# Optimization experiments

Measured on AMD Instinct MI355X. Metric: run time of the kernel, lower is better.

Reference implementation:

```python
import jax, jax.numpy as jnp
import numpy as np

B, SQ, SK, DK, DV = 16, 2048, 2048, 64, 64


def setup_inputs() -> dict:
    key = jax.random.key(0)
    kq, kk, kv, km = jax.random.split(key, 4)
    Q = jax.random.normal(kq, (B, SQ, DK), dtype=jnp.float32)
    K = jax.random.normal(kk, (B, SK, DK), dtype=jnp.float32)
    V = jax.random.normal(kv, (B, SK, DV), dtype=jnp.float32)
    mask = jax.random.randint(km, (B, 1, SK), 0, 2, dtype=jnp.int32)
    return {"Q": Q, "K": K, "V": V, "mask": mask}


def reference(Q, K, V, mask):
    d = K.shape[-1]
    # scores: (B, SQ, SK) -- full attention matrix, as in the torch module
    attn = jnp.einsum("bqd,bkd->bqk", Q, K) / (d ** 0.5)
    masked = mask == 0  # (B, 1, SK), broadcasts over query dim
    attn = jnp.where(masked, jnp.float32(-1e9), attn)
    attn = jax.nn.softmax(attn, axis=-1)
    attn = jnp.where(masked, jnp.float32(0.0), attn)
    output = jnp.einsum("bqk,bkv->bqv", attn, V)
    return (output, attn)
```

## Files before the change

kernel.cpp:

```cpp
#include <hip/hip_runtime.h>
#include <hip/hip_bf16.h>

#define NB   16
#define SQL  2048
#define SKL  2048
#define DKL  64
#define DVL  64
#define NE   (NB * SQL * DKL)

typedef __attribute__((ext_vector_type(8))) short short8;
typedef __attribute__((ext_vector_type(4))) short s16x4;
typedef __attribute__((ext_vector_type(4))) float f32x4;

#define VST 56
#define PST 56

#define SCALE_LOG2E 0.1803368801111204f
#define EXP2F(x) __builtin_amdgcn_exp2f(x)

__device__ __forceinline__ short f2bf(float x) {
    unsigned u = __builtin_bit_cast(unsigned, x);
    u = (u + 0x7fffu + ((u >> 16) & 1u)) >> 16;
    return (short)u;
}
__device__ __forceinline__ float bf2f(short s) {
    return __builtin_bit_cast(float, ((unsigned)(unsigned short)s) << 16);
}

__global__ __launch_bounds__(256)
void prep(const float* __restrict__ Q, const float* __restrict__ K,
          const float* __restrict__ V, short* __restrict__ ws)
{
    short* qhi = ws;
    short* qlo = ws + (size_t)NE;
    short* khi = ws + (size_t)2 * NE;
    short* klo = ws + (size_t)3 * NE;
    short* vb  = ws + (size_t)4 * NE;

    size_t i4 = ((size_t)blockIdx.x * 256 + threadIdx.x) * 4;
    if (i4 >= NE) return;

    f32x4 q = *(const f32x4*)(Q + i4);
    f32x4 k = *(const f32x4*)(K + i4);
    f32x4 v = *(const f32x4*)(V + i4);
    s16x4 qh, ql, kh, kl, vv;
    #pragma unroll
    for (int j = 0; j < 4; j++) {
        qh[j] = f2bf(q[j]);  ql[j] = f2bf(q[j] - bf2f(qh[j]));
        kh[j] = f2bf(k[j]);  kl[j] = f2bf(k[j] - bf2f(kh[j]));
        vv[j] = f2bf(v[j]);
    }
    *(s16x4*)(qhi + i4) = qh;
    *(s16x4*)(qlo + i4) = ql;
    *(s16x4*)(khi + i4) = kh;
    *(s16x4*)(klo + i4) = kl;
    *(s16x4*)(vb  + i4) = vv;
}

__device__ __forceinline__ void qk_tiles(const short* __restrict__ khi,
                                         const short* __restrict__ klo, int kb,
                                         int l15, int quad,
                                         short8 qa0h, short8 qa1h,
                                         short8 qa0l, short8 qa1l,
                                         f32x4& s0, f32x4& s1) {
    size_t o0 = (size_t)(kb + l15) * DKL + quad * 8;
    size_t o1 = (size_t)(kb + 16 + l15) * DKL + quad * 8;
    short8 h0l = *(const short8*)(khi + o0);
    short8 h0h = *(const short8*)(khi + o0 + 32);
    short8 h1l = *(const short8*)(khi + o1);
    short8 h1h = *(const short8*)(khi + o1 + 32);
    short8 l0l = *(const short8*)(klo + o0);
    short8 l0h = *(const short8*)(klo + o0 + 32);
    short8 l1l = *(const short8*)(klo + o1);
    short8 l1h = *(const short8*)(klo + o1 + 32);
    f32x4 z = {0.f, 0.f, 0.f, 0.f};
    s0 = __builtin_amdgcn_mfma_f32_16x16x32_bf16(qa0h, h0l, z, 0, 0, 0);
    s0 = __builtin_amdgcn_mfma_f32_16x16x32_bf16(qa1h, h0h, s0, 0, 0, 0);
    s0 = __builtin_amdgcn_mfma_f32_16x16x32_bf16(qa0h, l0l, s0, 0, 0, 0);
    s0 = __builtin_amdgcn_mfma_f32_16x16x32_bf16(qa1h, l0h, s0, 0, 0, 0);
    s0 = __builtin_amdgcn_mfma_f32_16x16x32_bf16(qa0l, h0l, s0, 0, 0, 0);
    s0 = __builtin_amdgcn_mfma_f32_16x16x32_bf16(qa1l, h0h, s0, 0, 0, 0);
    s1 = __builtin_amdgcn_mfma_f32_16x16x32_bf16(qa0h, h1l, z, 0, 0, 0);
    s1 = __builtin_amdgcn_mfma_f32_16x16x32_bf16(qa1h, h1h, s1, 0, 0, 0);
    s1 = __builtin_amdgcn_mfma_f32_16x16x32_bf16(qa0h, l1l, s1, 0, 0, 0);
    s1 = __builtin_amdgcn_mfma_f32_16x16x32_bf16(qa1h, l1h, s1, 0, 0, 0);
    s1 = __builtin_amdgcn_mfma_f32_16x16x32_bf16(qa0l, h1l, s1, 0, 0, 0);
    s1 = __builtin_amdgcn_mfma_f32_16x16x32_bf16(qa1l, h1h, s1, 0, 0, 0);
}

__global__ __launch_bounds__(256)
void attn_fwd(const short* __restrict__ ws, const int* __restrict__ mask,
              float* __restrict__ out, float* __restrict__ attn)
{
    __shared__ float s_bias[SKL];
    __shared__ short s_vt[64 * VST];
    __shared__ short s_p[4 * 16 * PST];

    const int tid  = threadIdx.x;
    const int wave = tid >> 6;
    const int l15  = tid & 15;
    const int quad = (tid & 63) >> 4;

    const int b     = blockIdx.x >> 5;
    const int qblk  = blockIdx.x & 31;
    const int qbase = qblk * 64 + wave * 16;

    for (int i = tid; i < SKL; i += 256)
        s_bias[i] = mask[b * SKL + i] ? 0.0f : -1e9f;
    __syncthreads();

    const short* qhi = ws +             (size_t)(b * SQL + qbase) * DKL;
    const short* qlo = ws + (size_t)NE + (size_t)(b * SQL + qbase) * DKL;
    const short* khi = ws + (size_t)2 * NE + (size_t)b * SKL * DKL;
    const short* klo = ws + (size_t)3 * NE + (size_t)b * SKL * DKL;
    const short* vb  = ws + (size_t)4 * NE + (size_t)b * SKL * DVL;

    short8 qa0h = *(const short8*)(qhi + (size_t)l15 * DKL + quad * 8);
    short8 qa1h = *(const short8*)(qhi + (size_t)l15 * DKL + 32 + quad * 8);
    short8 qa0l = *(const short8*)(qlo + (size_t)l15 * DKL + quad * 8);
    short8 qa1l = *(const short8*)(qlo + (size_t)l15 * DKL + 32 + quad * 8);

    float lsum[4] = {0.f, 0.f, 0.f, 0.f};
    for (int kb = 0; kb < SKL; kb += 32) {
        f32x4 s0, s1;
        qk_tiles(khi, klo, kb, l15, quad, qa0h, qa1h, qa0l, qa1l, s0, s1);
        float bias0 = s_bias[kb + l15];
        float bias1 = s_bias[kb + 16 + l15];
        #pragma unroll
        for (int r = 0; r < 4; r++) {
            lsum[r] += EXP2F(fmaf(s0[r], SCALE_LOG2E, bias0));
            lsum[r] += EXP2F(fmaf(s1[r], SCALE_LOG2E, bias1));
        }
    }
    #pragma unroll
    for (int off = 1; off <= 8; off <<= 1) {
        #pragma unroll
        for (int r = 0; r < 4; r++)
            lsum[r] += __shfl_xor(lsum[r], off, 64);
    }
    float inv_l[4];
    #pragma unroll
    for (int r = 0; r < 4; r++) inv_l[r] = 1.0f / lsum[r];

    f32x4 acc[4];
    #pragma unroll
    for (int vt = 0; vt < 4; vt++) { f32x4 z = {0.f,0.f,0.f,0.f}; acc[vt] = z; }

    const int vk  = tid & 31;
    const int vv0 = (tid >> 5) * 8;
    short* pw = s_p + wave * 16 * PST;

    for (int kb = 0; kb < SKL; kb += 32) {
        __syncthreads();
        {
            short8 vvv = *(const short8*)(vb + (size_t)(kb + vk) * DVL + vv0);
            #pragma unroll
            for (int j = 0; j < 8; j++)
                s_vt[(vv0 + j) * VST + vk] = vvv[j];
        }
        __syncthreads();

        f32x4 s0, s1;
        qk_tiles(khi, klo, kb, l15, quad, qa0h, qa1h, qa0l, qa1l, s0, s1);
        float bias0 = s_bias[kb + l15];
        float bias1 = s_bias[kb + 16 + l15];

        const size_t arow = (size_t)(b * SQL + qbase + quad * 4) * SKL + kb;
        #pragma unroll
        for (int r = 0; r < 4; r++) {
            float p0 = EXP2F(fmaf(s0[r], SCALE_LOG2E, bias0)) * inv_l[r];
            float p1 = EXP2F(fmaf(s1[r], SCALE_LOG2E, bias1)) * inv_l[r];
            attn[arow + (size_t)r * SKL + l15]      = p0;
            attn[arow + (size_t)r * SKL + 16 + l15] = p1;
            pw[(quad * 4 + r) * PST + l15]      = f2bf(p0);
            pw[(quad * 4 + r) * PST + 16 + l15] = f2bf(p1);
        }

        short8 pa = *(const short8*)(pw + l15 * PST + quad * 8);
        #pragma unroll
        for (int vt = 0; vt < 4; vt++) {
            short8 bvv = *(const short8*)(s_vt + (vt * 16 + l15) * VST + quad * 8);
            acc[vt] = __builtin_amdgcn_mfma_f32_16x16x32_bf16(pa, bvv, acc[vt], 0, 0, 0);
        }
    }

    #pragma unroll
    for (int vt = 0; vt < 4; vt++) {
        #pragma unroll
        for (int r = 0; r < 4; r++)
            out[(size_t)(b * SQL + qbase + quad * 4 + r) * DVL + vt * 16 + l15] =
                acc[vt][r];
    }
}

extern "C" void kernel_launch(void* const* d_in, const int* in_sizes, int n_in,
                              void* d_out, int out_size, void* d_ws, size_t ws_size,
                              hipStream_t stream) {
    const float* Q    = (const float*)d_in[0];
    const float* K    = (const float*)d_in[1];
    const float* V    = (const float*)d_in[2];
    const int*   mask = (const int*)d_in[3];
    float* out  = (float*)d_out;
    float* attn = out + (size_t)NB * SQL * DVL;
    short* ws   = (short*)d_ws;

    prep<<<dim3(NE / (256 * 4)), dim3(256), 0, stream>>>(Q, K, V, ws);
    attn_fwd<<<dim3(NB * (SQL / 64)), dim3(256), 0, stream>>>(ws, mask, out, attn);
}
```

Baseline: 523.7 us.

## Split key range across waves, pretranspose V globally, drop per-tile LDS syncs

```diff
diff --git a/kernel.cpp b/kernel.cpp
--- a/kernel.cpp
+++ b/kernel.cpp
@@ -1,5 +1,4 @@
 #include <hip/hip_runtime.h>
-#include <hip/hip_bf16.h>
 
 #define NB   16
 #define SQL  2048
@@ -12,7 +11,6 @@
 typedef __attribute__((ext_vector_type(4))) short s16x4;
 typedef __attribute__((ext_vector_type(4))) float f32x4;
 
-#define VST 56
 #define PST 56
 
 #define SCALE_LOG2E 0.1803368801111204f
@@ -29,32 +27,59 @@
 
 __global__ __launch_bounds__(256)
 void prep(const float* __restrict__ Q, const float* __restrict__ K,
-          const float* __restrict__ V, short* __restrict__ ws)
+          short* __restrict__ ws)
 {
     short* qhi = ws;
     short* qlo = ws + (size_t)NE;
     short* khi = ws + (size_t)2 * NE;
     short* klo = ws + (size_t)3 * NE;
-    short* vb  = ws + (size_t)4 * NE;
 
     size_t i4 = ((size_t)blockIdx.x * 256 + threadIdx.x) * 4;
     if (i4 >= NE) return;
 
     f32x4 q = *(const f32x4*)(Q + i4);
     f32x4 k = *(const f32x4*)(K + i4);
-    f32x4 v = *(const f32x4*)(V + i4);
-    s16x4 qh, ql, kh, kl, vv;
+    s16x4 qh, ql, kh, kl;
     #pragma unroll
     for (int j = 0; j < 4; j++) {
         qh[j] = f2bf(q[j]);  ql[j] = f2bf(q[j] - bf2f(qh[j]));
         kh[j] = f2bf(k[j]);  kl[j] = f2bf(k[j] - bf2f(kh[j]));
-        vv[j] = f2bf(v[j]);
     }
     *(s16x4*)(qhi + i4) = qh;
     *(s16x4*)(qlo + i4) = ql;
     *(s16x4*)(khi + i4) = kh;
     *(s16x4*)(klo + i4) = kl;
-    *(s16x4*)(vb  + i4) = vv;
+}
+
+__global__ __launch_bounds__(256)
+void vtrans(const float* __restrict__ V, short* __restrict__ vt)
+{
+    __shared__ short st[64][72];
+    const int b  = blockIdx.x >> 5;
+    const int kt = blockIdx.x & 31;
+    const int t  = threadIdx.x;
+
+    const int kr = t >> 2;
+    const int c0 = (t & 3) * 16;
+    const float* vsrc = V + ((size_t)(b * SKL) + kt * 64 + kr) * DVL + c0;
+    #pragma unroll
+    for (int j = 0; j < 4; j++) {
+        f32x4 x = *(const f32x4*)(vsrc + j * 4);
+        #pragma unroll
+        for (int i = 0; i < 4; i++) st[kr][c0 + j * 4 + i] = f2bf(x[i]);
+    }
+    __syncthreads();
+
+    const int vr = t >> 2;
+    const int k0 = (t & 3) * 16;
+    short* dst = vt + (size_t)b * DVL * SKL + (size_t)vr * SKL + kt * 64 + k0;
+    #pragma unroll
+    for (int j = 0; j < 4; j++) {
+        s16x4 o;
+        #pragma unroll
+        for (int m = 0; m < 4; m++) o[m] = st[k0 + j * 4 + m][vr];
+        *(s16x4*)(dst + j * 4) = o;
+    }
 }
 
 __device__ __forceinline__ void qk_tiles(const short* __restrict__ khi,
@@ -88,32 +113,35 @@
     s1 = __builtin_amdgcn_mfma_f32_16x16x32_bf16(qa1l, h1h, s1, 0, 0, 0);
 }
 
-__global__ __launch_bounds__(256)
+__global__ __launch_bounds__(256, 4)
 void attn_fwd(const short* __restrict__ ws, const int* __restrict__ mask,
               float* __restrict__ out, float* __restrict__ attn)
 {
-    __shared__ float s_bias[SKL];
-    __shared__ short s_vt[64 * VST];
-    __shared__ short s_p[4 * 16 * PST];
+    __shared__ __align__(16) char smem[16384 + 256];
+    short* s_p   = (short*)smem;
+    f32x4* s_acc = (f32x4*)smem;
+    float* s_red = (float*)(smem + 16384);
 
     const int tid  = threadIdx.x;
-    const int wave = tid >> 6;
+    const int w    = tid >> 6;
+    const int lane = tid & 63;
     const int l15  = tid & 15;
     const int quad = (tid & 63) >> 4;
 
-    const int b     = blockIdx.x >> 5;
-    const int qblk  = blockIdx.x & 31;
-    const int qbase = qblk * 64 + wave * 16;
-
-    for (int i = tid; i < SKL; i += 256)
-        s_bias[i] = mask[b * SKL + i] ? 0.0f : -1e9f;
-    __syncthreads();
-
-    const short* qhi = ws +             (size_t)(b * SQL + qbase) * DKL;
-    const short* qlo = ws + (size_t)NE + (size_t)(b * SQL + qbase) * DKL;
+    const int bid = blockIdx.x;
+    const int swz = (bid & 7) * ((NB * SQL / 16) >> 3) + (bid >> 3);
+    const int b     = swz >> 7;
+    const int qbase = (swz & 127) * 16;
+
+    const int k0 = w * (SKL / 4);
+    const int k1 = k0 + SKL / 4;
+
+    const short* qhi = ws + (size_t)(b * SQL + qbase) * DKL;
+    const short* qlo = qhi + (size_t)NE;
     const short* khi = ws + (size_t)2 * NE + (size_t)b * SKL * DKL;
-    const short* klo = ws + (size_t)3 * NE + (size_t)b * SKL * DKL;
-    const short* vb  = ws + (size_t)4 * NE + (size_t)b * SKL * DVL;
+    const short* klo = khi + (size_t)NE;
+    const short* vtg = ws + (size_t)4 * NE + (size_t)b * DVL * SKL;
+    const int*   mk  = mask + b * SKL;
 
     short8 qa0h = *(const short8*)(qhi + (size_t)l15 * DKL + quad * 8);
     short8 qa1h = *(const short8*)(qhi + (size_t)l15 * DKL + 32 + quad * 8);
@@ -121,11 +149,11 @@
     short8 qa1l = *(const short8*)(qlo + (size_t)l15 * DKL + 32 + quad * 8);
 
     float lsum[4] = {0.f, 0.f, 0.f, 0.f};
-    for (int kb = 0; kb < SKL; kb += 32) {
+    for (int kb = k0; kb < k1; kb += 32) {
         f32x4 s0, s1;
         qk_tiles(khi, klo, kb, l15, quad, qa0h, qa1h, qa0l, qa1l, s0, s1);
-        float bias0 = s_bias[kb + l15];
-        float bias1 = s_bias[kb + 16 + l15];
+        float bias0 = mk[kb + l15]      ? 0.0f : -1e9f;
+        float bias1 = mk[kb + 16 + l15] ? 0.0f : -1e9f;
         #pragma unroll
         for (int r = 0; r < 4; r++) {
             lsum[r] += EXP2F(fmaf(s0[r], SCALE_LOG2E, bias0));
@@ -138,59 +166,70 @@
         for (int r = 0; r < 4; r++)
             lsum[r] += __shfl_xor(lsum[r], off, 64);
     }
+    if (l15 == 0) {
+        #pragma unroll
+        for (int r = 0; r < 4; r++) s_red[w * 16 + quad * 4 + r] = lsum[r];
+    }
+    __syncthreads();
     float inv_l[4];
     #pragma unroll
-    for (int r = 0; r < 4; r++) inv_l[r] = 1.0f / lsum[r];
+    for (int r = 0; r < 4; r++) {
+        float t_ = s_red[quad * 4 + r] + s_red[16 + quad * 4 + r]
+                 + s_red[32 + quad * 4 + r] + s_red[48 + quad * 4 + r];
+        inv_l[r] = 1.0f / t_;
+    }
 
     f32x4 acc[4];
     #pragma unroll
     for (int vt = 0; vt < 4; vt++) { f32x4 z = {0.f,0.f,0.f,0.f}; acc[vt] = z; }
 
-    const int vk  = tid & 31;
-    const int vv0 = (tid >> 5) * 8;
-    short* pw = s_p + wave * 16 * PST;
-
-    for (int kb = 0; kb < SKL; kb += 32) {
-        __syncthreads();
-        {
-            short8 vvv = *(const short8*)(vb + (size_t)(kb + vk) * DVL + vv0);
-            #pragma unroll
-            for (int j = 0; j < 8; j++)
-                s_vt[(vv0 + j) * VST + vk] = vvv[j];
-        }
-        __syncthreads();
+    short* pw = s_p + w * 16 * PST;
+
+    for (int kb = k0; kb < k1; kb += 32) {
+        const short* vrow = vtg + kb + quad * 8;
+        short8 bv0 = *(const short8*)(vrow + (size_t)(0 * 16 + l15) * SKL);
+        short8 bv1 = *(const short8*)(vrow + (size_t)(1 * 16 + l15) * SKL);
+        short8 bv2 = *(const short8*)(vrow + (size_t)(2 * 16 + l15) * SKL);
+        short8 bv3 = *(const short8*)(vrow + (size_t)(3 * 16 + l15) * SKL);
+        float bias0 = mk[kb + l15]      ? 0.0f : -1e9f;
+        float bias1 = mk[kb + 16 + l15] ? 0.0f : -1e9f;
 
         f32x4 s0, s1;
         qk_tiles(khi, klo, kb, l15, quad, qa0h, qa1h, qa0l, qa1l, s0, s1);
-        float bias0 = s_bias[kb + l15];
-        float bias1 = s_bias[kb + 16 + l15];
 
         const size_t arow = (size_t)(b * SQL + qbase + quad * 4) * SKL + kb;
         #pragma unroll
         for (int r = 0; r < 4; r++) {
             float p0 = EXP2F(fmaf(s0[r], SCALE_LOG2E, bias0)) * inv_l[r];
             float p1 = EXP2F(fmaf(s1[r], SCALE_LOG2E, bias1)) * inv_l[r];
-            attn[arow + (size_t)r * SKL + l15]      = p0;
-            attn[arow + (size_t)r * SKL + 16 + l15] = p1;
+            __builtin_nontemporal_store(p0, &attn[arow + (size_t)r * SKL + l15]);
+            __builtin_nontemporal_store(p1, &attn[arow + (size_t)r * SKL + 16 + l15]);
             pw[(quad * 4 + r) * PST + l15]      = f2bf(p0);
             pw[(quad * 4 + r) * PST + 16 + l15] = f2bf(p1);
         }
 
         short8 pa = *(const short8*)(pw + l15 * PST + quad * 8);
-        #pragma unroll
-        for (int vt = 0; vt < 4; vt++) {
-            short8 bvv = *(const short8*)(s_vt + (vt * 16 + l15) * VST + quad * 8);
-            acc[vt] = __builtin_amdgcn_mfma_f32_16x16x32_bf16(pa, bvv, acc[vt], 0, 0, 0);
-        }
-    }
-
-    #pragma unroll
-    for (int vt = 0; vt < 4; vt++) {
-        #pragma unroll
-        for (int r = 0; r < 4; r++)
-            out[(size_t)(b * SQL + qbase + quad * 4 + r) * DVL + vt * 16 + l15] =
-                acc[vt][r];
-    }
+        acc[0] = __builtin_amdgcn_mfma_f32_16x16x32_bf16(pa, bv0, acc[0], 0, 0, 0);
+        acc[1] = __builtin_amdgcn_mfma_f32_16x16x32_bf16(pa, bv1, acc[1], 0, 0, 0);
+        acc[2] = __builtin_amdgcn_mfma_f32_16x16x32_bf16(pa, bv2, acc[2], 0, 0, 0);
+        acc[3] = __builtin_amdgcn_mfma_f32_16x16x32_bf16(pa, bv3, acc[3], 0, 0, 0);
+    }
+
+    __syncthreads();
+    #pragma unroll
+    for (int vt = 0; vt < 4; vt++) s_acc[(w * 64 + lane) * 4 + vt] = acc[vt];
+    __syncthreads();
+
+    f32x4 t_ = s_acc[(0 * 64 + lane) * 4 + w];
+    #pragma unroll
+    for (int wp = 1; wp < 4; wp++) {
+        f32x4 u = s_acc[(wp * 64 + lane) * 4 + w];
+        #pragma unroll
+        for (int r = 0; r < 4; r++) t_[r] += u[r];
+    }
+    #pragma unroll
+    for (int r = 0; r < 4; r++)
+        out[(size_t)(b * SQL + qbase + quad * 4 + r) * DVL + w * 16 + l15] = t_[r];
 }
 
 extern "C" void kernel_launch(void* const* d_in, const int* in_sizes, int n_in,
@@ -204,6 +243,7 @@
     float* attn = out + (size_t)NB * SQL * DVL;
     short* ws   = (short*)d_ws;
 
-    prep<<<dim3(NE / (256 * 4)), dim3(256), 0, stream>>>(Q, K, V, ws);
-    attn_fwd<<<dim3(NB * (SQL / 64)), dim3(256), 0, stream>>>(ws, mask, out, attn);
-}
+    prep<<<dim3(NE / (256 * 4)), dim3(256), 0, stream>>>(Q, K, ws);
+    vtrans<<<dim3(NB * (SKL / 64)), dim3(256), 0, stream>>>(V, ws + (size_t)4 * NE);
+    attn_fwd<<<dim3(NB * (SQL / 16)), dim3(256), 0, stream>>>(ws, mask, out, attn);
+}
```

New measurement: 550.8 us. 1.05x slower.
